# Performance work log

Hardware: AMD Instinct MI355X
Metric: run time of the kernel (lower is better)

## Reference

```python
import jax, jax.numpy as jnp
import numpy as np

L, B, E, H = 512, 4, 512, 8
D = E // H  # head_dim = 64


def setup_inputs() -> dict:
    key = jax.random.key(0)
    ks = jax.random.split(key, 7)
    query = jax.random.normal(ks[0], (L, B, E), dtype=jnp.float32)
    relation_k = jax.random.normal(ks[1], (B, L, L, D), dtype=jnp.float32)
    relation_v = jax.random.normal(ks[2], (B, L, L, D), dtype=jnp.float32)
    # xavier-uniform-ish scale for the fused QKV projection
    lim = float(np.sqrt(6.0 / (3 * E + E)))
    in_proj_weight = jax.random.uniform(ks[3], (3 * E, E), jnp.float32, -lim, lim)
    in_proj_bias = jnp.zeros((3 * E,), jnp.float32)
    lim_o = float(np.sqrt(1.0 / E))
    out_proj_weight = jax.random.uniform(ks[4], (E, E), jnp.float32, -lim_o, lim_o)
    out_proj_bias = jnp.zeros((E,), jnp.float32)
    return {
        "query": query,
        "relation_k": relation_k,
        "relation_v": relation_v,
        "in_proj_weight": in_proj_weight,
        "in_proj_bias": in_proj_bias,
        "out_proj_weight": out_proj_weight,
        "out_proj_bias": out_proj_bias,
    }


def reference(query, relation_k, relation_v, in_proj_weight, in_proj_bias,
              out_proj_weight, out_proj_bias):
    # query == key == value (qkv_same path), shape (L, B, E)
    scaling = float(D) ** -0.5
    qkv = query @ in_proj_weight.T + in_proj_bias          # (L, B, 3E)
    q, k, v = jnp.split(qkv, 3, axis=-1)                   # each (L, B, E)
    q = q * scaling

    def to_bhld(t):  # (L, B, E) -> (B, H, L, D)
        return t.reshape(L, B, H, D).transpose(1, 2, 0, 3)

    q, k, v = to_bhld(q), to_bhld(k), to_bhld(v)

    # content scores
    scores = jnp.einsum('bhid,bhjd->bhij', q, k)           # (B, H, L, L)

    # relation_k term: torch does a flat .view of (B*H, L, L, D) -> (B*H*L, D, L)
    # which is a row-major REINTERPRETATION (not a transpose). Replicate via reshape:
    rk = relation_k.reshape(B, L, D, L)                    # per-(b,i) block (L*D,) -> (D, L)
    scores = scores + jnp.einsum('bhid,bidj->bhij', q, rk)

    w = jax.nn.softmax(scores, axis=-1)
    w = jnp.where(jnp.isnan(w), jnp.zeros_like(w), w)      # NaN guard as in original

    out = jnp.einsum('bhij,bhjd->bhid', w, v)              # (B, H, L, D)
    # relation_v term: (B*H*L, 1, L) @ (B*H*L, L, D) -> per-query weighted relation values
    out = out + jnp.einsum('bhij,bijd->bhid', w, relation_v)

    out = out.transpose(2, 0, 1, 3).reshape(L, B, E)       # (B,H,L,D) -> (L,B,E)
    return out @ out_proj_weight.T + out_proj_bias
```

## Files before the change

kernel.cpp:

```cpp
#include <hip/hip_runtime.h>
#include <hip/hip_fp16.h>
#include <stdint.h>


typedef short short8 __attribute__((ext_vector_type(8)));
typedef float f32x4 __attribute__((ext_vector_type(4)));
typedef unsigned short u16x4 __attribute__((ext_vector_type(4)));

static __device__ __forceinline__ uint16_t f2bf(float f) {
  uint32_t u = __float_as_uint(f);
  uint32_t r = (u + 0x7FFFu + ((u >> 16) & 1u)) >> 16;
  return (uint16_t)r;
}
static __device__ __forceinline__ float bf2f(uint16_t h) {
  return __uint_as_float(((uint32_t)h) << 16);
}
static __device__ __forceinline__ short8 ld8(const uint16_t* p) {
  return *(const short8*)p;
}
#define MFMA(a, b, c) __builtin_amdgcn_mfma_f32_16x16x32_bf16((a), (b), (c), 0, 0, 0)

__global__ __launch_bounds__(256) void k_conv_all(
    const float* __restrict__ in_w, const float* __restrict__ query,
    const float* __restrict__ out_w, uint16_t* __restrict__ w_hi,
    uint16_t* __restrict__ w_lo, uint16_t* __restrict__ a_hi,
    uint16_t* __restrict__ a_lo, uint16_t* __restrict__ wo_bf) {
  int e = (blockIdx.x * 256 + threadIdx.x) * 4;
  if (e < 786432) {
    f32x4 v = *(const f32x4*)(in_w + e);
    u16x4 hi, lo;
#pragma unroll
    for (int k = 0; k < 4; ++k) {
      hi[k] = f2bf(v[k]);
      lo[k] = f2bf(v[k] - bf2f(hi[k]));
    }
    *(u16x4*)(w_hi + e) = hi;
    *(u16x4*)(w_lo + e) = lo;
  } else if (e < 786432 + 1048576) {
    int o = e - 786432;
    f32x4 v = *(const f32x4*)(query + o);
    u16x4 hi, lo;
#pragma unroll
    for (int k = 0; k < 4; ++k) {
      hi[k] = f2bf(v[k]);
      lo[k] = f2bf(v[k] - bf2f(hi[k]));
    }
    *(u16x4*)(a_hi + o) = hi;
    *(u16x4*)(a_lo + o) = lo;
  } else {
    int o = e - 1835008;
    f32x4 v = *(const f32x4*)(out_w + o);
    u16x4 hi;
#pragma unroll
    for (int k = 0; k < 4; ++k) hi[k] = f2bf(v[k]);
    *(u16x4*)(wo_bf + o) = hi;
  }
}

__global__ __launch_bounds__(256) void k_inproj(
    const uint16_t* __restrict__ a_hi, const uint16_t* __restrict__ a_lo,
    const uint16_t* __restrict__ w_hi, const uint16_t* __restrict__ w_lo,
    const float* __restrict__ bias, float* __restrict__ q_s,
    uint16_t* __restrict__ q_bf, uint16_t* __restrict__ k_bf,
    uint16_t* __restrict__ v_bf) {
  const int wave = threadIdx.x >> 6, lane = threadIdx.x & 63;
  const int wr = wave >> 1, wc = wave & 1;
  const int rif = lane & 15, kg = lane >> 4;
  const int rbase = blockIdx.x * 64 + wr * 32;
  const int cbase = blockIdx.y * 64 + wc * 32;
  f32x4 acc[2][2] = {};
  for (int ks = 0; ks < 512; ks += 32) {
    int kofs = ks + kg * 8;
    short8 aH[2], aL[2], bH[2], bL[2];
#pragma unroll
    for (int m = 0; m < 2; ++m) {
      size_t idx = (size_t)(rbase + m * 16 + rif) * 512 + kofs;
      aH[m] = ld8(a_hi + idx);
      aL[m] = ld8(a_lo + idx);
    }
#pragma unroll
    for (int n = 0; n < 2; ++n) {
      size_t idx = (size_t)(cbase + n * 16 + rif) * 512 + kofs;
      bH[n] = ld8(w_hi + idx);
      bL[n] = ld8(w_lo + idx);
    }
#pragma unroll
    for (int m = 0; m < 2; ++m)
#pragma unroll
      for (int n = 0; n < 2; ++n) {
        acc[m][n] = MFMA(aH[m], bH[n], acc[m][n]);
        acc[m][n] = MFMA(aH[m], bL[n], acc[m][n]);
        acc[m][n] = MFMA(aL[m], bH[n], acc[m][n]);
      }
  }
#pragma unroll
  for (int m = 0; m < 2; ++m)
#pragma unroll
    for (int n = 0; n < 2; ++n)
#pragma unroll
      for (int r = 0; r < 4; ++r) {
        int row = rbase + m * 16 + kg * 4 + r;
        int col = cbase + n * 16 + rif;
        float val = acc[m][n][r] + bias[col];
        int l = row >> 2, b = row & 3;
        int sel = col >> 9, h = (col >> 6) & 7, d = col & 63;
        size_t oidx = ((size_t)(b * 8 + h) * 512 + l) * 64 + d;
        if (sel == 0) {
          val *= 0.125f;
          q_s[oidx] = val;
          q_bf[oidx] = f2bf(val);
        } else if (sel == 1) {
          k_bf[oidx] = f2bf(val);
        } else {
          v_bf[oidx] = f2bf(val);
        }
      }
}

__global__ __launch_bounds__(256) void k_scores(const uint16_t* __restrict__ q_bf,
                                                const uint16_t* __restrict__ k_bf,
                                                __half* __restrict__ scores) {
  const int bh = blockIdx.x;
  const uint16_t* qb = q_bf + (size_t)bh * 512 * 64;
  const uint16_t* kb = k_bf + (size_t)bh * 512 * 64;
  const int wave = threadIdx.x >> 6, lane = threadIdx.x & 63;
  const int wr = wave >> 1, wc = wave & 1;
  const int rif = lane & 15, kg = lane >> 4;
  const int ibase = blockIdx.y * 64 + wr * 32;
  const int jbase = blockIdx.z * 64 + wc * 32;
  f32x4 acc[2][2] = {};
#pragma unroll
  for (int ks = 0; ks < 64; ks += 32) {
    int kofs = ks + kg * 8;
    short8 A[2], Bb[2];
#pragma unroll
    for (int m = 0; m < 2; ++m) A[m] = ld8(qb + (size_t)(ibase + m * 16 + rif) * 64 + kofs);
#pragma unroll
    for (int n = 0; n < 2; ++n) Bb[n] = ld8(kb + (size_t)(jbase + n * 16 + rif) * 64 + kofs);
#pragma unroll
    for (int m = 0; m < 2; ++m)
#pragma unroll
      for (int n = 0; n < 2; ++n) acc[m][n] = MFMA(A[m], Bb[n], acc[m][n]);
  }
  __half* sc = scores + (size_t)bh * 512 * 512;
#pragma unroll
  for (int m = 0; m < 2; ++m)
#pragma unroll
    for (int n = 0; n < 2; ++n)
#pragma unroll
      for (int r = 0; r < 4; ++r)
        sc[(size_t)(ibase + m * 16 + kg * 4 + r) * 512 + (jbase + n * 16 + rif)] =
            __float2half(acc[m][n][r]);
}

__global__ __launch_bounds__(256) void k_rksm2(
    const float* __restrict__ relation_k, const float* __restrict__ q_s,
    const __half* __restrict__ scores, uint16_t* __restrict__ wprob) {
  __shared__ float qh[512];
  __shared__ float shr[4608];
  const int b = blockIdx.x >> 9, i = blockIdx.x & 511;
  const int t = threadIdx.x;
  const int wave = t >> 6, lane = t & 63;
  for (int e = t; e < 512; e += 256) {
    int h = e >> 6, d = e & 63;
    qh[d * 8 + h] = q_s[(((size_t)b * 8 + h) * 512 + i) * 64 + d];
  }
  __syncthreads();
  const int H = wave & 1, Dh = wave >> 1;
  const int j0 = H * 256 + lane * 4;
  f32x4 acc[8];
#pragma unroll
  for (int h = 0; h < 8; ++h) acc[h] = f32x4{0.f, 0.f, 0.f, 0.f};
  {
    const float* rkp =
        relation_k + ((size_t)b * 512 + i) * 32768 + (size_t)Dh * 32 * 512 + j0;
    const float* qp = qh + Dh * 32 * 8;
    for (int dd = 0; dd < 32; dd += 8) {
      f32x4 kv[8];
#pragma unroll
      for (int u = 0; u < 8; ++u)
        kv[u] = __builtin_nontemporal_load((const f32x4*)(rkp + (size_t)(dd + u) * 512));
#pragma unroll
      for (int u = 0; u < 8; ++u) {
        f32x4 qA = *(const f32x4*)(qp + (dd + u) * 8);
        f32x4 qB = *(const f32x4*)(qp + (dd + u) * 8 + 4);
#pragma unroll
        for (int h = 0; h < 4; ++h) {
          acc[h] += qA[h] * kv[u];
          acc[4 + h] += qB[h] * kv[u];
        }
      }
    }
  }
  if (Dh == 1) {
#pragma unroll
    for (int h = 0; h < 8; ++h)
      *(f32x4*)&shr[(H * 64 + lane) * 33 + h * 4] = acc[h];
  }
  __syncthreads();
  if (Dh == 0) {
#pragma unroll
    for (int h = 0; h < 8; ++h)
      acc[h] += *(const f32x4*)&shr[(H * 64 + lane) * 33 + h * 4];
  }
  __syncthreads();
  if (Dh == 0) {
#pragma unroll
    for (int h = 0; h < 8; ++h) *(f32x4*)&shr[h * 512 + j0] = acc[h];
  }
  __syncthreads();
#pragma unroll
  for (int hh = 0; hh < 2; ++hh) {
    int h = wave * 2 + hh;
    const __half* srow = scores + (((size_t)b * 8 + h) * 512 + i) * 512;
    float s[8], m = -1e30f;
#pragma unroll
    for (int jj = 0; jj < 8; ++jj) {
      int j = jj * 64 + lane;
      s[jj] = __half2float(srow[j]) + shr[h * 512 + j];
      m = fmaxf(m, s[jj]);
    }
    for (int o = 32; o > 0; o >>= 1) m = fmaxf(m, __shfl_xor(m, o));
    float ex[8], sum = 0.f;
#pragma unroll
    for (int jj = 0; jj < 8; ++jj) {
      ex[jj] = __expf(s[jj] - m);
      sum += ex[jj];
    }
    for (int o = 32; o > 0; o >>= 1) sum += __shfl_xor(sum, o);
    float r = 1.f / sum;
    uint16_t* wrow = wprob + (((size_t)b * 8 + h) * 512 + i) * 512;
#pragma unroll
    for (int jj = 0; jj < 8; ++jj) wrow[jj * 64 + lane] = f2bf(ex[jj] * r);
  }
}

__global__ __launch_bounds__(256) void k_pv(const uint16_t* __restrict__ w_bf,
                                            const uint16_t* __restrict__ v_bf,
                                            uint16_t* __restrict__ pv_bf) {
  const int bh = blockIdx.x;
  const int b = bh >> 3, h = bh & 7;
  const uint16_t* wb = w_bf + (size_t)bh * 512 * 512;
  const uint16_t* vb = v_bf + (size_t)bh * 512 * 64;
  const int wave = threadIdx.x >> 6, lane = threadIdx.x & 63;
  const int wr = wave >> 1, wc = wave & 1;
  const int rif = lane & 15, kg = lane >> 4;
  const int ibase = blockIdx.y * 64 + wr * 32;
  const int dbase = wc * 32;
  f32x4 acc[2][2] = {};
  for (int ks = 0; ks < 512; ks += 32) {
    int kofs = ks + kg * 8;
    short8 A[2], Bb[2];
#pragma unroll
    for (int m = 0; m < 2; ++m) A[m] = ld8(wb + (size_t)(ibase + m * 16 + rif) * 512 + kofs);
#pragma unroll
    for (int n = 0; n < 2; ++n) {
      uint16_t tb[8];
#pragma unroll
      for (int e = 0; e < 8; ++e) tb[e] = vb[(size_t)(kofs + e) * 64 + dbase + n * 16 + rif];
      Bb[n] = *(const short8*)tb;
    }
#pragma unroll
    for (int m = 0; m < 2; ++m)
#pragma unroll
      for (int n = 0; n < 2; ++n) acc[m][n] = MFMA(A[m], Bb[n], acc[m][n]);
  }
#pragma unroll
  for (int m = 0; m < 2; ++m)
#pragma unroll
    for (int n = 0; n < 2; ++n)
#pragma unroll
      for (int r = 0; r < 4; ++r) {
        int i = ibase + m * 16 + kg * 4 + r;
        int d = dbase + n * 16 + rif;
        pv_bf[((size_t)i * 4 + b) * 512 + h * 64 + d] = f2bf(acc[m][n][r]);
      }
}

__global__ __launch_bounds__(256) void k_rv2(const float* __restrict__ relation_v,
                                             const uint16_t* __restrict__ wprob,
                                             uint16_t* __restrict__ rv_bf) {
  __shared__ float wT[4608];
  const int b = blockIdx.x >> 9, i = blockIdx.x & 511;
  const int t = threadIdx.x;
  const int wave = t >> 6, lane = t & 63;
  for (int jj = t; jj < 512; jj += 256) {
    uint16_t tmp[8];
#pragma unroll
    for (int h = 0; h < 8; ++h)
      tmp[h] = wprob[(((size_t)b * 8 + h) * 512 + i) * 512 + jj];
#pragma unroll
    for (int h = 0; h < 8; ++h) wT[jj * 9 + h] = bf2f(tmp[h]);
  }
  __syncthreads();
  f32x4 racc[8];
#pragma unroll
  for (int h = 0; h < 8; ++h) racc[h] = f32x4{0.f, 0.f, 0.f, 0.f};
  {
    const int jsub = lane >> 4, d4 = (lane & 15) * 4;
    const float* rvb = relation_v + ((size_t)b * 512 + i) * 32768;
    for (int s8 = 0; s8 < 32; s8 += 8) {
      f32x4 rvv[8];
      int js[8];
#pragma unroll
      for (int u = 0; u < 8; ++u) {
        js[u] = (s8 + u) * 16 + wave * 4 + jsub;
        rvv[u] = *(const f32x4*)(rvb + (size_t)js[u] * 64 + d4);
      }
#pragma unroll
      for (int u = 0; u < 8; ++u) {
        f32x4 w0 = *(const f32x4*)&wT[js[u] * 9];
        f32x4 w1 = *(const f32x4*)&wT[js[u] * 9 + 4];
#pragma unroll
        for (int h = 0; h < 4; ++h) {
          racc[h] += w0[h] * rvv[u];
          racc[4 + h] += w1[h] * rvv[u];
        }
      }
    }
  }
#pragma unroll
  for (int h = 0; h < 8; ++h)
#pragma unroll
    for (int c = 0; c < 4; ++c) {
      racc[h][c] += __shfl_xor(racc[h][c], 16);
      racc[h][c] += __shfl_xor(racc[h][c], 32);
    }
  __syncthreads();
  if (lane < 16) {
#pragma unroll
    for (int h = 0; h < 8; ++h)
      *(f32x4*)&wT[(wave * 8 + h) * 64 + (lane & 15) * 4] = racc[h];
  }
  __syncthreads();
  for (int e = t; e < 512; e += 256) {
    int h = e >> 6, d = e & 63;
    float s = wT[(0 * 8 + h) * 64 + d] + wT[(1 * 8 + h) * 64 + d] +
              wT[(2 * 8 + h) * 64 + d] + wT[(3 * 8 + h) * 64 + d];
    rv_bf[((size_t)i * 4 + b) * 512 + h * 64 + d] = f2bf(s);
  }
}

__global__ __launch_bounds__(256) void k_outproj(const uint16_t* __restrict__ rv_a,
                                                 const uint16_t* __restrict__ pv_a,
                                                 const uint16_t* __restrict__ wo_bf,
                                                 const float* __restrict__ bias,
                                                 float* __restrict__ out) {
  const int wave = threadIdx.x >> 6, lane = threadIdx.x & 63;
  const int wr = wave >> 1, wc = wave & 1;
  const int rif = lane & 15, kg = lane >> 4;
  const int rbase = blockIdx.x * 64 + wr * 32;
  const int cbase = blockIdx.y * 64 + wc * 32;
  f32x4 acc[2][2] = {};
  for (int ks = 0; ks < 512; ks += 32) {
    int kofs = ks + kg * 8;
    short8 A[2], Bb[2];
#pragma unroll
    for (int m = 0; m < 2; ++m) {
      size_t idx = (size_t)(rbase + m * 16 + rif) * 512 + kofs;
      short8 p = ld8(pv_a + idx);
      short8 rr = ld8(rv_a + idx);
      uint16_t tb[8];
#pragma unroll
      for (int e = 0; e < 8; ++e)
        tb[e] = f2bf(bf2f((uint16_t)p[e]) + bf2f((uint16_t)rr[e]));
      A[m] = *(const short8*)tb;
    }
#pragma unroll
    for (int n = 0; n < 2; ++n) Bb[n] = ld8(wo_bf + (size_t)(cbase + n * 16 + rif) * 512 + kofs);
#pragma unroll
    for (int m = 0; m < 2; ++m)
#pragma unroll
      for (int n = 0; n < 2; ++n) acc[m][n] = MFMA(A[m], Bb[n], acc[m][n]);
  }
#pragma unroll
  for (int m = 0; m < 2; ++m)
#pragma unroll
    for (int n = 0; n < 2; ++n)
#pragma unroll
      for (int r = 0; r < 4; ++r) {
        int row = rbase + m * 16 + kg * 4 + r;
        int col = cbase + n * 16 + rif;
        out[(size_t)row * 512 + col] = acc[m][n][r] + bias[col];
      }
}

extern "C" void kernel_launch(void* const* d_in, const int* in_sizes, int n_in,
                              void* d_out, int out_size, void* d_ws, size_t ws_size,
                              hipStream_t stream) {
  const float* query = (const float*)d_in[0];
  const float* relation_k = (const float*)d_in[1];
  const float* relation_v = (const float*)d_in[2];
  const float* in_w = (const float*)d_in[3];
  const float* in_b = (const float*)d_in[4];
  const float* out_w = (const float*)d_in[5];
  const float* out_b = (const float*)d_in[6];
  float* out = (float*)d_out;
  char* ws = (char*)d_ws;

  uint16_t* a_hi  = (uint16_t*)(ws + 0);
  uint16_t* a_lo  = (uint16_t*)(ws + 2097152);
  uint16_t* w_hi  = (uint16_t*)(ws + 4194304);
  uint16_t* w_lo  = (uint16_t*)(ws + 5767168);
  uint16_t* wo_bf = (uint16_t*)(ws + 7340032);
  float*    q_s   = (float*)   (ws + 7864320);
  uint16_t* q_bf  = (uint16_t*)(ws + 12058624);
  uint16_t* k_bf  = (uint16_t*)(ws + 14155776);
  uint16_t* v_bf  = (uint16_t*)(ws + 16252928);
  uint16_t* rv_bf = (uint16_t*)(ws + 18350080);
  uint16_t* pv_bf = (uint16_t*)(ws + 20447232);
  uint16_t* wprob = (uint16_t*)(ws + 22544384);
  __half*   sc_h  = (__half*)  (ws + 39321600);

  k_conv_all<<<dim3(2048), 256, 0, stream>>>(in_w, query, out_w, w_hi, w_lo, a_hi, a_lo, wo_bf);
  k_inproj<<<dim3(32, 24), 256, 0, stream>>>(a_hi, a_lo, w_hi, w_lo, in_b, q_s, q_bf, k_bf, v_bf);
  k_scores<<<dim3(32, 8, 8), 256, 0, stream>>>(q_bf, k_bf, sc_h);
  k_rksm2<<<dim3(2048), 256, 0, stream>>>(relation_k, q_s, sc_h, wprob);
  k_pv<<<dim3(32, 8), 256, 0, stream>>>(wprob, v_bf, pv_bf);
  k_rv2<<<dim3(2048), 256, 0, stream>>>(relation_v, wprob, rv_bf);
  k_outproj<<<dim3(32, 8), 256, 0, stream>>>(rv_bf, pv_bf, wo_bf, out_b, out);
}
```

Baseline: 198.0 us.

## Fuse QK content scores into relation-K softmax kernel using transposed fp32 K

Removes the separate bf16 MFMA scores kernel and its fp16 score buffer. The relation-K kernel now also accumulates q·k directly in fp32 from a transposed K layout written by the in-projection. This avoids writing and rereading a B*H*L*L fp16 scores tensor and saves a launch. In exchange it adds extra per-block global reads of K, 8 heads per j-chunk, using scalar FMA instead of tensor cores, and halves the relation_k load batch.

```diff
diff --git a/kernel.cpp b/kernel.cpp
--- a/kernel.cpp
+++ b/kernel.cpp
@@ -1,5 +1,4 @@
 #include <hip/hip_runtime.h>
-#include <hip/hip_fp16.h>
 #include <stdint.h>
 
 
@@ -61,8 +60,7 @@
     const uint16_t* __restrict__ a_hi, const uint16_t* __restrict__ a_lo,
     const uint16_t* __restrict__ w_hi, const uint16_t* __restrict__ w_lo,
     const float* __restrict__ bias, float* __restrict__ q_s,
-    uint16_t* __restrict__ q_bf, uint16_t* __restrict__ k_bf,
-    uint16_t* __restrict__ v_bf) {
+    float* __restrict__ kT, uint16_t* __restrict__ v_bf) {
   const int wave = threadIdx.x >> 6, lane = threadIdx.x & 63;
   const int wr = wave >> 1, wc = wave & 1;
   const int rif = lane & 15, kg = lane >> 4;
@@ -104,58 +102,20 @@
         float val = acc[m][n][r] + bias[col];
         int l = row >> 2, b = row & 3;
         int sel = col >> 9, h = (col >> 6) & 7, d = col & 63;
-        size_t oidx = ((size_t)(b * 8 + h) * 512 + l) * 64 + d;
         if (sel == 0) {
           val *= 0.125f;
-          q_s[oidx] = val;
-          q_bf[oidx] = f2bf(val);
+          q_s[(((size_t)b * 8 + h) * 512 + l) * 64 + d] = val;
         } else if (sel == 1) {
-          k_bf[oidx] = f2bf(val);
+          kT[(((size_t)b * 8 + h) * 64 + d) * 512 + l] = val;
         } else {
-          v_bf[oidx] = f2bf(val);
+          v_bf[(((size_t)b * 8 + h) * 512 + l) * 64 + d] = f2bf(val);
         }
       }
 }
 
-__global__ __launch_bounds__(256) void k_scores(const uint16_t* __restrict__ q_bf,
-                                                const uint16_t* __restrict__ k_bf,
-                                                __half* __restrict__ scores) {
-  const int bh = blockIdx.x;
-  const uint16_t* qb = q_bf + (size_t)bh * 512 * 64;
-  const uint16_t* kb = k_bf + (size_t)bh * 512 * 64;
-  const int wave = threadIdx.x >> 6, lane = threadIdx.x & 63;
-  const int wr = wave >> 1, wc = wave & 1;
-  const int rif = lane & 15, kg = lane >> 4;
-  const int ibase = blockIdx.y * 64 + wr * 32;
-  const int jbase = blockIdx.z * 64 + wc * 32;
-  f32x4 acc[2][2] = {};
-#pragma unroll
-  for (int ks = 0; ks < 64; ks += 32) {
-    int kofs = ks + kg * 8;
-    short8 A[2], Bb[2];
-#pragma unroll
-    for (int m = 0; m < 2; ++m) A[m] = ld8(qb + (size_t)(ibase + m * 16 + rif) * 64 + kofs);
-#pragma unroll
-    for (int n = 0; n < 2; ++n) Bb[n] = ld8(kb + (size_t)(jbase + n * 16 + rif) * 64 + kofs);
-#pragma unroll
-    for (int m = 0; m < 2; ++m)
-#pragma unroll
-      for (int n = 0; n < 2; ++n) acc[m][n] = MFMA(A[m], Bb[n], acc[m][n]);
-  }
-  __half* sc = scores + (size_t)bh * 512 * 512;
-#pragma unroll
-  for (int m = 0; m < 2; ++m)
-#pragma unroll
-    for (int n = 0; n < 2; ++n)
-#pragma unroll
-      for (int r = 0; r < 4; ++r)
-        sc[(size_t)(ibase + m * 16 + kg * 4 + r) * 512 + (jbase + n * 16 + rif)] =
-            __float2half(acc[m][n][r]);
-}
-
-__global__ __launch_bounds__(256) void k_rksm2(
-    const float* __restrict__ relation_k, const float* __restrict__ q_s,
-    const __half* __restrict__ scores, uint16_t* __restrict__ wprob) {
+__global__ __launch_bounds__(256) void k_rksm2p(
+    const float* __restrict__ relation_k, const float* __restrict__ kT,
+    const float* __restrict__ q_s, uint16_t* __restrict__ wprob) {
   __shared__ float qh[512];
   __shared__ float shr[4608];
   const int b = blockIdx.x >> 9, i = blockIdx.x & 511;
@@ -174,16 +134,31 @@
   {
     const float* rkp =
         relation_k + ((size_t)b * 512 + i) * 32768 + (size_t)Dh * 32 * 512 + j0;
+    const float* ktp = kT + (size_t)b * 262144 + (size_t)Dh * 32 * 512 + j0;
     const float* qp = qh + Dh * 32 * 8;
-    for (int dd = 0; dd < 32; dd += 8) {
-      f32x4 kv[8];
-#pragma unroll
-      for (int u = 0; u < 8; ++u)
-        kv[u] = __builtin_nontemporal_load((const f32x4*)(rkp + (size_t)(dd + u) * 512));
-#pragma unroll
-      for (int u = 0; u < 8; ++u) {
-        f32x4 qA = *(const f32x4*)(qp + (dd + u) * 8);
-        f32x4 qB = *(const f32x4*)(qp + (dd + u) * 8 + 4);
+    for (int dd0 = 0; dd0 < 32; dd0 += 4) {
+      f32x4 kv[4];
+#pragma unroll
+      for (int u = 0; u < 4; ++u)
+        kv[u] = __builtin_nontemporal_load((const f32x4*)(rkp + (size_t)(dd0 + u) * 512));
+#pragma unroll
+      for (int u = 0; u < 4; ++u) {
+        int dd = dd0 + u;
+        f32x4 qA = *(const f32x4*)(qp + dd * 8);
+        f32x4 qB = *(const f32x4*)(qp + dd * 8 + 4);
+#pragma unroll
+        for (int h = 0; h < 4; ++h) {
+          f32x4 ktv0 = *(const f32x4*)(ktp + (size_t)h * 32768 + (size_t)dd * 512);
+          f32x4 ktv1 = *(const f32x4*)(ktp + (size_t)(h + 4) * 32768 + (size_t)dd * 512);
+          acc[h] += qA[h] * ktv0;
+          acc[4 + h] += qB[h] * ktv1;
+        }
+      }
+#pragma unroll
+      for (int u = 0; u < 4; ++u) {
+        int dd = dd0 + u;
+        f32x4 qA = *(const f32x4*)(qp + dd * 8);
+        f32x4 qB = *(const f32x4*)(qp + dd * 8 + 4);
 #pragma unroll
         for (int h = 0; h < 4; ++h) {
           acc[h] += qA[h] * kv[u];
@@ -212,12 +187,10 @@
 #pragma unroll
   for (int hh = 0; hh < 2; ++hh) {
     int h = wave * 2 + hh;
-    const __half* srow = scores + (((size_t)b * 8 + h) * 512 + i) * 512;
     float s[8], m = -1e30f;
 #pragma unroll
     for (int jj = 0; jj < 8; ++jj) {
-      int j = jj * 64 + lane;
-      s[jj] = __half2float(srow[j]) + shr[h * 512 + j];
+      s[jj] = shr[h * 512 + jj * 64 + lane];
       m = fmaxf(m, s[jj]);
     }
     for (int o = 32; o > 0; o >>= 1) m = fmaxf(m, __shfl_xor(m, o));
@@ -404,18 +377,15 @@
   uint16_t* w_lo  = (uint16_t*)(ws + 5767168);
   uint16_t* wo_bf = (uint16_t*)(ws + 7340032);
   float*    q_s   = (float*)   (ws + 7864320);
-  uint16_t* q_bf  = (uint16_t*)(ws + 12058624);
-  uint16_t* k_bf  = (uint16_t*)(ws + 14155776);
+  float*    kT    = (float*)   (ws + 12058624);
   uint16_t* v_bf  = (uint16_t*)(ws + 16252928);
   uint16_t* rv_bf = (uint16_t*)(ws + 18350080);
   uint16_t* pv_bf = (uint16_t*)(ws + 20447232);
   uint16_t* wprob = (uint16_t*)(ws + 22544384);
-  __half*   sc_h  = (__half*)  (ws + 39321600);
 
   k_conv_all<<<dim3(2048), 256, 0, stream>>>(in_w, query, out_w, w_hi, w_lo, a_hi, a_lo, wo_bf);
-  k_inproj<<<dim3(32, 24), 256, 0, stream>>>(a_hi, a_lo, w_hi, w_lo, in_b, q_s, q_bf, k_bf, v_bf);
-  k_scores<<<dim3(32, 8, 8), 256, 0, stream>>>(q_bf, k_bf, sc_h);
-  k_rksm2<<<dim3(2048), 256, 0, stream>>>(relation_k, q_s, sc_h, wprob);
+  k_inproj<<<dim3(32, 24), 256, 0, stream>>>(a_hi, a_lo, w_hi, w_lo, in_b, q_s, kT, v_bf);
+  k_rksm2p<<<dim3(2048), 256, 0, stream>>>(relation_k, kT, q_s, wprob);
   k_pv<<<dim3(32, 8), 256, 0, stream>>>(wprob, v_bf, pv_bf);
   k_rv2<<<dim3(2048), 256, 0, stream>>>(relation_v, wprob, rv_bf);
   k_outproj<<<dim3(32, 8), 256, 0, stream>>>(rv_bf, pv_bf, wo_bf, out_b, out);
```

After: 251.2 us. 26.9% more time.
